# Kernel tuning notes

Measured on AMD Instinct MI355X. Metric: run time of the kernel, lower is better.

Reference implementation:

```python
import jax, jax.numpy as jnp
import numpy as np

C_IN, C_OUT = 256, 128

def setup_inputs() -> dict:
    key = jax.random.key(0)
    k1, k2, k3, k4, k5, k6 = jax.random.split(key, 6)
    B, H, W = 8, 64, 64
    p = jax.random.normal(k1, (B, C_IN, H, W), dtype=jnp.float32)
    b = jax.random.normal(k2, (B, C_IN, H, W), dtype=jnp.float32)
    # 1x1 conv weights (Conv2d with kernel 1 == pointwise matmul) + biases
    sq = 1.0 / np.sqrt(C_IN)
    Wq = jax.random.uniform(k3, (C_OUT, C_IN), jnp.float32, -sq, sq)
    bq = jax.random.uniform(k4, (C_OUT,), jnp.float32, -sq, sq)
    Wk = jax.random.uniform(k5, (C_OUT, C_IN), jnp.float32, -sq, sq)
    bk = jax.random.uniform(k6, (C_OUT,), jnp.float32, -sq, sq)
    return {"p": p, "b": b, "Wq": Wq, "bq": bq, "Wk": Wk, "bk": bk}

def reference(p, b, Wq, bq, Wk, bk):
    B, C, H, W = p.shape
    N = H * W
    # 1x1 convs -> flatten spatial dim to N
    q = jnp.einsum('bchw,oc->bhwo', p, Wq) + bq          # [B,H,W,Co]
    q = q.reshape(B, N, -1).astype(jnp.float32)           # [B,N,Co] (query permuted)
    k = jnp.einsum('bchw,oc->bohw', b, Wk) + bk[None, :, None, None]
    k = k.reshape(B, -1, N).astype(jnp.float32)           # [B,Co,N]
    energy = jnp.einsum('bnc,bcm->bnm', q, k)             # [B,N,N] unscaled
    attention = jax.nn.softmax(energy, axis=-1)           # softmax over keys
    value = b.reshape(B, C, N)                            # [B,C,N]
    out = jnp.einsum('bnm,bcm->bcn', attention, value)    # [B,C,N]
    return out.reshape(B, C, H, W)
```

## Files before the change

### kernel.cpp

```cpp
#include <hip/hip_runtime.h>
#include <hip/hip_bf16.h>
#include <math.h>


#define B_   8
#define CIN  256
#define COUT 128
#define NN   4096

typedef _Float16 half8  __attribute__((ext_vector_type(8)));
typedef short    short8 __attribute__((ext_vector_type(8)));
typedef float    f32x4  __attribute__((ext_vector_type(4)));

#define LOG2E 1.44269504088896340736f

__device__ __forceinline__ unsigned short f2bf(float f) {
    union { float f; unsigned u; } v; v.f = f;
    return (unsigned short)((v.u + 0x7FFFu + ((v.u >> 16) & 1u)) >> 16);
}
__device__ __forceinline__ unsigned short f2h(float f) {
    union { _Float16 h; unsigned short u; } v; v.h = (_Float16)f;
    return v.u;
}
__device__ __forceinline__ unsigned int cvt_pk_bf16(float lo, float hi) {
    unsigned int r;
    asm("v_cvt_pk_bf16_f32 %0, %1, %2" : "=v"(r) : "v"(lo), "v"(hi));
    return r;
}
__device__ __forceinline__ float dpp_xor1(float x) {
    union { float f; int i; } u; u.f = x;
    u.i = __builtin_amdgcn_mov_dpp(u.i, 0xB1, 0xF, 0xF, true);
    return u.f;
}
__device__ __forceinline__ void dma16(void* lds, const void* g) {
    __builtin_amdgcn_global_load_lds(
        (const __attribute__((address_space(1))) unsigned int*)g,
        (__attribute__((address_space(3))) unsigned int*)lds,
        16, 0, 0);
}

__global__ __launch_bounds__(256) void cvt_w(const float* __restrict__ Wq,
                                             const float* __restrict__ Wk,
                                             const float* __restrict__ bq,
                                             _Float16* __restrict__ Whq,
                                             _Float16* __restrict__ Whk,
                                             float* __restrict__ bqs) {
    const int bx = blockIdx.x, t = threadIdx.x;
    const int isK = (bx >= 32);
    const float* src = isK ? Wk : Wq;
    _Float16* dst = isK ? Whk : Whq;
    const float scale = isK ? 1.0f : LOG2E;
    const int idx = (bx & 31) * 256 + t;
    float4 v = ((const float4*)src)[idx];
    unsigned long long pk = (unsigned long long)f2h(v.x * scale)
                          | ((unsigned long long)f2h(v.y * scale) << 16)
                          | ((unsigned long long)f2h(v.z * scale) << 32)
                          | ((unsigned long long)f2h(v.w * scale) << 48);
    ((unsigned long long*)dst)[idx] = pk;
    if (bx == 0 && t < COUT) bqs[t] = bq[t] * LOG2E;
}

__global__ __launch_bounds__(256) void proj3(const float* __restrict__ X,
                                             const _Float16* __restrict__ Wh,
                                             const float* __restrict__ bias,
                                             _Float16* __restrict__ outN,
                                             _Float16* __restrict__ outT,
                                             unsigned short* __restrict__ Vb)
{
    __shared__ __align__(16) unsigned short T[64 * 264];
    const int bx = blockIdx.x, b = bx >> 6, n0 = (bx & 63) << 6;
    const int t  = threadIdx.x;
    const int cr = t >> 2;
    const int nch = (t & 3) << 4;

#pragma unroll
    for (int it = 0; it < 4; ++it) {
        const int c = it * 64 + cr;
        const float* src = X + ((size_t)(b * CIN + c) * NN + n0 + nch);
        float v[16];
#pragma unroll
        for (int k = 0; k < 4; ++k) {
            float4 f = *(const float4*)(src + k * 4);
            v[k*4] = f.x; v[k*4+1] = f.y; v[k*4+2] = f.z; v[k*4+3] = f.w;
        }
#pragma unroll
        for (int j = 0; j < 16; ++j) T[(nch + j) * 264 + c] = f2h(v[j]);
        if (Vb) {
            unsigned short o[16];
#pragma unroll
            for (int j = 0; j < 16; ++j) o[j] = f2bf(v[j]);
            unsigned short* dst = Vb + (size_t)(b * CIN + c) * NN + n0 + nch;
            *(int4*)dst = *(int4*)o;
            *(int4*)(dst + 8) = *(int4*)(o + 8);
        }
    }
    __syncthreads();

    const int w = t >> 6, lane = t & 63, l15 = lane & 15, quad = lane >> 4, q8 = quad * 8;
    half8 a[8];
#pragma unroll
    for (int s = 0; s < 8; ++s)
        a[s] = *(const half8*)&T[(w * 16 + l15) * 264 + s * 32 + q8];
    f32x4 D[8];
#pragma unroll
    for (int og = 0; og < 8; ++og) D[og] = (f32x4){0.f, 0.f, 0.f, 0.f};
#pragma unroll
    for (int s = 0; s < 8; ++s) {
        const _Float16* wp = Wh + (size_t)l15 * CIN + s * 32 + q8;
#pragma unroll
        for (int og = 0; og < 8; ++og) {
            half8 wf = *(const half8*)(wp + og * 16 * CIN);
            D[og] = __builtin_amdgcn_mfma_f32_16x16x32_f16(a[s], wf, D[og], 0, 0, 0);
        }
    }
    const int nrow = n0 + w * 16 + quad * 4;
    if (outT) {
#pragma unroll
        for (int og = 0; og < 8; ++og) {
            const int o = og * 16 + l15;
            const float bo = bias[o];
            const int c = o >> 3, j = o & 7;
            const int sw = (c & 7) << 2;
#pragma unroll
            for (int r2 = 0; r2 < 4; ++r2) {
                const int n = nrow + r2;
                const int tile = n >> 5, m = n & 31;
                const size_t pos = ((size_t)(b * 128 + tile) * 512
                                    + c * 32 + ((m + sw) & 31)) * 8 + j;
                outT[pos] = (_Float16)(D[og][r2] + bo);
            }
        }
    } else {
#pragma unroll
        for (int og = 0; og < 8; ++og) {
            const int o = og * 16 + l15;
            const float bo = bias[o];
            _Float16* op = outN + ((size_t)(b * NN + nrow) * COUT + o);
#pragma unroll
            for (int r2 = 0; r2 < 4; ++r2)
                op[(size_t)r2 * COUT] = (_Float16)(D[og][r2] + bo);
        }
    }
}

__global__ __launch_bounds__(256, 2) void flash_kernel(const _Float16* __restrict__ Q,
                                                       const _Float16* __restrict__ Ktt,
                                                       const unsigned short* __restrict__ V,
                                                       float* __restrict__ out) {
    __shared__ __align__(16) _Float16       K0sh[32 * 128];
    __shared__ __align__(16) _Float16       K1sh[32 * 128];
    __shared__ __align__(16) unsigned short V0sh[256 * 32];
    __shared__ __align__(16) unsigned short V1sh[256 * 32];
    __shared__ __align__(16) unsigned short V2sh[256 * 32];
    __shared__ __align__(16) unsigned short P0sh[64 * 40];
    __shared__ __align__(16) unsigned short P1sh[64 * 40];
    __shared__ __align__(16) float          Lsh[64];

    const int bx   = blockIdx.x;
    const int b    = bx >> 6;
    const int q0   = (bx & 63) << 6;
    const int t    = threadIdx.x;
    const int w    = t >> 6;
    const int lane = t & 63;
    const int l15  = lane & 15;
    const int quad = lane >> 4;
    const int q8   = quad * 8;

    const _Float16* Qg = Q + (size_t)b * NN * COUT;
    const _Float16* Kb = Ktt + (size_t)b * 128 * 4096;
    const unsigned short* Vg = V + (size_t)b * CIN * NN;

    half8 Qf[4];
    {
        const _Float16* qr = Qg + (size_t)(q0 + w * 16 + l15) * COUT;
#pragma unroll
        for (int s = 0; s < 4; ++s)
            Qf[s] = *(const half8*)(qr + s * 32 + q8);
    }

    f32x4 O[16];
#pragma unroll
    for (int i = 0; i < 16; ++i) O[i] = (f32x4){0.f, 0.f, 0.f, 0.f};
    float lsum[4] = {0.f, 0.f, 0.f, 0.f};

    const int vmq   = ((lane & 3) - ((lane >> 3) & 3)) & 3;
    const int vcrow = lane >> 2;
    const int vslot = (quad + (l15 >> 1)) & 3;

    auto issueK = [&](int kt, _Float16* Kd) {
        const _Float16* gk = Kb + (size_t)kt * 4096;
        dma16(Kd + (w * 2 + 0) * 512, gk + (w * 2 + 0) * 512 + lane * 8);
        dma16(Kd + (w * 2 + 1) * 512, gk + (w * 2 + 1) * 512 + lane * 8);
    };
    auto issueV = [&](int kt, unsigned short* Vd) {
        const int k0 = kt << 5;
#pragma unroll
        for (int i = 0; i < 4; ++i) {
            const int cc = (w * 4 + i) * 16 + vcrow;
            dma16(Vd + (w * 4 + i) * 512,
                  Vg + (size_t)cc * NN + k0 + vmq * 8);
        }
    };

    auto halfstep = [&](int kt, const _Float16* Kc, _Float16* Kn,
                        const unsigned short* Va, unsigned short* Vn2,
                        unsigned short* Pc) {
        if (kt + 1 < 128) issueK(kt + 1, Kn);

        f32x4 S0 = {0.f, 0.f, 0.f, 0.f}, S1 = {0.f, 0.f, 0.f, 0.f};
        __builtin_amdgcn_s_setprio(1);
#pragma unroll
        for (int s = 0; s < 4; ++s) {
            const int kc = 4 * s + quad;
            const int sw = (kc & 7) << 2;
            const int x0 = (l15 + sw) & 31;
            half8 kf0 = *(const half8*)(Kc + (kc * 32 + x0) * 8);
            half8 kf1 = *(const half8*)(Kc + (kc * 32 + (x0 ^ 16)) * 8);
            S0 = __builtin_amdgcn_mfma_f32_16x16x32_f16(Qf[s], kf0, S0, 0, 0, 0);
            S1 = __builtin_amdgcn_mfma_f32_16x16x32_f16(Qf[s], kf1, S1, 0, 0, 0);
        }
        __builtin_amdgcn_s_setprio(0);

        f32x4 E0, E1;
#pragma unroll
        for (int r = 0; r < 4; ++r) {
            E0[r] = exp2f(S0[r]);
            E1[r] = exp2f(S1[r]);
            lsum[r] += E0[r] + E1[r];
        }
        {
            f32x4 P0, P1;
#pragma unroll
            for (int r = 0; r < 4; ++r) { P0[r] = dpp_xor1(E0[r]); P1[r] = dpp_xor1(E1[r]); }
            const int odd = l15 & 1;
            unsigned short* wp0 = Pc + w * 640
                                + (((quad << 2) + (odd << 1)) * 40) + (l15 & ~1);
            unsigned int pk0 = cvt_pk_bf16(odd ? P0[2] : E0[0], odd ? E0[2] : P0[0]);
            unsigned int pk1 = cvt_pk_bf16(odd ? P0[3] : E0[1], odd ? E0[3] : P0[1]);
            unsigned int pk2 = cvt_pk_bf16(odd ? P1[2] : E1[0], odd ? E1[2] : P1[0]);
            unsigned int pk3 = cvt_pk_bf16(odd ? P1[3] : E1[1], odd ? E1[3] : P1[1]);
            *(unsigned int*)&wp0[0]  = pk0;
            *(unsigned int*)&wp0[40] = pk1;
            *(unsigned int*)&wp0[16] = pk2;
            *(unsigned int*)&wp0[56] = pk3;
        }

        __syncthreads();

        if (kt + 2 < 128) issueV(kt + 2, Vn2);

        {
            short8 pf[4];
#pragma unroll
            for (int ni = 0; ni < 4; ++ni)
                pf[ni] = *(const short8*)(Pc + (ni * 16 + l15) * 40 + q8);
            const unsigned short* vb = Va + (w * 64 + l15) * 32 + vslot * 8;
            __builtin_amdgcn_s_setprio(1);
#pragma unroll
            for (int cj = 0; cj < 4; ++cj) {
                short8 vf = *(const short8*)(vb + cj * 512);
#pragma unroll
                for (int ni = 0; ni < 4; ++ni)
                    O[ni * 4 + cj] = __builtin_amdgcn_mfma_f32_16x16x32_bf16(pf[ni], vf, O[ni * 4 + cj], 0, 0, 0);
            }
            __builtin_amdgcn_s_setprio(0);
        }
    };

    issueK(0, K0sh);
    issueV(0, V0sh);
    issueV(1, V1sh);
    __syncthreads();

    _Float16*       Kc = K0sh; _Float16*       Kn = K1sh;
    unsigned short* Va = V0sh; unsigned short* Vm = V1sh; unsigned short* Vn2 = V2sh;
    unsigned short* Pc = P0sh; unsigned short* Pn = P1sh;
#pragma unroll 1
    for (int kt = 0; kt < 128; ++kt) {
        halfstep(kt, Kc, Kn, Va, Vn2, Pc);
        _Float16* tk = Kc; Kc = Kn; Kn = tk;
        unsigned short* tv = Va; Va = Vm; Vm = Vn2; Vn2 = tv;
        unsigned short* tp = Pc; Pc = Pn; Pn = tp;
    }

#pragma unroll
    for (int r = 0; r < 4; ++r) {
        float s = lsum[r];
        s += __shfl_xor(s, 1);
        s += __shfl_xor(s, 2);
        s += __shfl_xor(s, 4);
        s += __shfl_xor(s, 8);
        if (l15 == 0) Lsh[w * 16 + (quad << 2) + r] = s;
    }
    __syncthreads();
    float* ob = out + (size_t)b * CIN * NN + q0;
#pragma unroll
    for (int ni = 0; ni < 4; ++ni) {
        const f32x4 lv = *(const f32x4*)&Lsh[ni * 16 + (quad << 2)];
        f32x4 linv;
#pragma unroll
        for (int r = 0; r < 4; ++r) linv[r] = 1.0f / lv[r];
        const int nb = ni * 16 + (quad << 2);
#pragma unroll
        for (int cj = 0; cj < 4; ++cj) {
            const int c = w * 64 + cj * 16 + l15;
            f32x4 val = O[ni * 4 + cj];
#pragma unroll
            for (int r = 0; r < 4; ++r) val[r] *= linv[r];
            *(f32x4*)(ob + (size_t)c * NN + nb) = val;
        }
    }
}

extern "C" void kernel_launch(void* const* d_in, const int* in_sizes, int n_in,
                              void* d_out, int out_size, void* d_ws, size_t ws_size,
                              hipStream_t stream) {
    const float* p  = (const float*)d_in[0];
    const float* bv = (const float*)d_in[1];
    const float* Wq = (const float*)d_in[2];
    const float* bq = (const float*)d_in[3];
    const float* Wk = (const float*)d_in[4];
    const float* bk = (const float*)d_in[5];
    float* outp = (float*)d_out;

    char* ws = (char*)d_ws;
    const size_t szQ = (size_t)B_ * NN * COUT * 2;
    const size_t szV = (size_t)B_ * NN * CIN * 2;
    const size_t szW = (size_t)COUT * CIN * 2;
    _Float16*       Qh  = (_Float16*)ws;
    _Float16*       Ktt = (_Float16*)(ws + szQ);
    unsigned short* Vb  = (unsigned short*)(ws + 2 * szQ);
    _Float16*       Whq = (_Float16*)(ws + 2 * szQ + szV);
    _Float16*       Whk = (_Float16*)(ws + 2 * szQ + szV + szW);
    float*          bqs = (float*)(ws + 2 * szQ + szV + 2 * szW);

    cvt_w<<<64, 256, 0, stream>>>(Wq, Wk, bq, Whq, Whk, bqs);
    proj3<<<512, 256, 0, stream>>>(p,  Whq, bqs, Qh, (_Float16*)nullptr, (unsigned short*)nullptr);
    proj3<<<512, 256, 0, stream>>>(bv, Whk, bk,  (_Float16*)nullptr, Ktt, Vb);
    flash_kernel<<<512, 256, 0, stream>>>(Qh, Ktt, Vb, outp);
}
```

Measured before the change: 284.4 us.

## Load V directly into registers, deepen K ring, stage projection stores through LDS

The flash kernel no longer DMAs V tiles into LDS. Each lane loads its V fragments straight from global memory into registers, double-buffered across two unrolled steps, while K uses a four-deep LDS ring and P uses four buffers. The projection kernel stages its outputs in LDS and writes them back with coalesced 16-byte stores, and it converts V to bf16 with the packed hardware instruction. These changes cut LDS traffic and scattered global stores, at the cost of more registers and uncoalesced per-lane V global loads.

```diff
diff --git a/kernel.cpp b/kernel.cpp
--- a/kernel.cpp
+++ b/kernel.cpp
@@ -14,10 +14,6 @@
 
 #define LOG2E 1.44269504088896340736f
 
-__device__ __forceinline__ unsigned short f2bf(float f) {
-    union { float f; unsigned u; } v; v.f = f;
-    return (unsigned short)((v.u + 0x7FFFu + ((v.u >> 16) & 1u)) >> 16);
-}
 __device__ __forceinline__ unsigned short f2h(float f) {
     union { _Float16 h; unsigned short u; } v; v.h = (_Float16)f;
     return v.u;
@@ -86,12 +82,12 @@
 #pragma unroll
         for (int j = 0; j < 16; ++j) T[(nch + j) * 264 + c] = f2h(v[j]);
         if (Vb) {
-            unsigned short o[16];
-#pragma unroll
-            for (int j = 0; j < 16; ++j) o[j] = f2bf(v[j]);
+            unsigned int o2[8];
+#pragma unroll
+            for (int j = 0; j < 8; ++j) o2[j] = cvt_pk_bf16(v[2*j], v[2*j+1]);
             unsigned short* dst = Vb + (size_t)(b * CIN + c) * NN + n0 + nch;
-            *(int4*)dst = *(int4*)o;
-            *(int4*)(dst + 8) = *(int4*)(o + 8);
+            *(int4*)dst = *(int4*)&o2[0];
+            *(int4*)(dst + 8) = *(int4*)&o2[4];
         }
     }
     __syncthreads();
@@ -113,8 +109,10 @@
             D[og] = __builtin_amdgcn_mfma_f32_16x16x32_f16(a[s], wf, D[og], 0, 0, 0);
         }
     }
-    const int nrow = n0 + w * 16 + quad * 4;
+    __syncthreads();
+
     if (outT) {
+        const int nrow = w * 16 + quad * 4;
 #pragma unroll
         for (int og = 0; og < 8; ++og) {
             const int o = og * 16 + l15;
@@ -124,22 +122,33 @@
 #pragma unroll
             for (int r2 = 0; r2 < 4; ++r2) {
                 const int n = nrow + r2;
-                const int tile = n >> 5, m = n & 31;
-                const size_t pos = ((size_t)(b * 128 + tile) * 512
-                                    + c * 32 + ((m + sw) & 31)) * 8 + j;
-                outT[pos] = (_Float16)(D[og][r2] + bo);
+                const int tl = n >> 5, m = n & 31;
+                T[tl * 4096 + (c * 32 + ((m + sw) & 31)) * 8 + j] = f2h(D[og][r2] + bo);
             }
         }
+        __syncthreads();
+        _Float16* dstk = outT + ((size_t)(b * 128 + (n0 >> 5)) * 4096 + t * 32);
+        const unsigned short* srck = T + t * 32;
+#pragma unroll
+        for (int k = 0; k < 4; ++k)
+            ((int4*)dstk)[k] = ((const int4*)srck)[k];
     } else {
+        const int nrow = w * 16 + quad * 4;
 #pragma unroll
         for (int og = 0; og < 8; ++og) {
             const int o = og * 16 + l15;
             const float bo = bias[o];
-            _Float16* op = outN + ((size_t)(b * NN + nrow) * COUT + o);
 #pragma unroll
             for (int r2 = 0; r2 < 4; ++r2)
-                op[(size_t)r2 * COUT] = (_Float16)(D[og][r2] + bo);
-        }
+                T[(nrow + r2) * 136 + o] = f2h(D[og][r2] + bo);
+        }
+        __syncthreads();
+        const int n = t >> 2, seg = t & 3;
+        const unsigned short* srcp = T + n * 136 + seg * 32;
+        _Float16* dstp = outN + ((size_t)(b * NN + n0 + n) * COUT + seg * 32);
+#pragma unroll
+        for (int k = 0; k < 4; ++k)
+            ((int4*)dstp)[k] = ((const int4*)srcp)[k];
     }
 }
 
@@ -147,13 +156,8 @@
                                                        const _Float16* __restrict__ Ktt,
                                                        const unsigned short* __restrict__ V,
                                                        float* __restrict__ out) {
-    __shared__ __align__(16) _Float16       K0sh[32 * 128];
-    __shared__ __align__(16) _Float16       K1sh[32 * 128];
-    __shared__ __align__(16) unsigned short V0sh[256 * 32];
-    __shared__ __align__(16) unsigned short V1sh[256 * 32];
-    __shared__ __align__(16) unsigned short V2sh[256 * 32];
-    __shared__ __align__(16) unsigned short P0sh[64 * 40];
-    __shared__ __align__(16) unsigned short P1sh[64 * 40];
+    __shared__ __align__(16) _Float16       Ksh[4 * 32 * 128];
+    __shared__ __align__(16) unsigned short Psh[4 * 64 * 40];
     __shared__ __align__(16) float          Lsh[64];
 
     const int bx   = blockIdx.x;
@@ -183,30 +187,23 @@
     for (int i = 0; i < 16; ++i) O[i] = (f32x4){0.f, 0.f, 0.f, 0.f};
     float lsum[4] = {0.f, 0.f, 0.f, 0.f};
 
-    const int vmq   = ((lane & 3) - ((lane >> 3) & 3)) & 3;
-    const int vcrow = lane >> 2;
-    const int vslot = (quad + (l15 >> 1)) & 3;
-
-    auto issueK = [&](int kt, _Float16* Kd) {
+    const unsigned short* Vlane = Vg + (size_t)(w * 64 + l15) * NN + q8;
+    short8 VA[4], VB[4];
+
+    auto issueK = [&](int kt) {
+        _Float16* Kd = Ksh + (size_t)(kt & 3) * 4096;
         const _Float16* gk = Kb + (size_t)kt * 4096;
         dma16(Kd + (w * 2 + 0) * 512, gk + (w * 2 + 0) * 512 + lane * 8);
         dma16(Kd + (w * 2 + 1) * 512, gk + (w * 2 + 1) * 512 + lane * 8);
     };
-    auto issueV = [&](int kt, unsigned short* Vd) {
-        const int k0 = kt << 5;
-#pragma unroll
-        for (int i = 0; i < 4; ++i) {
-            const int cc = (w * 4 + i) * 16 + vcrow;
-            dma16(Vd + (w * 4 + i) * 512,
-                  Vg + (size_t)cc * NN + k0 + vmq * 8);
-        }
+    auto loadV = [&](int kt, short8* Vd) {
+#pragma unroll
+        for (int cj = 0; cj < 4; ++cj)
+            Vd[cj] = *(const short8*)(Vlane + (size_t)cj * 16 * NN + kt * 32);
     };
 
-    auto halfstep = [&](int kt, const _Float16* Kc, _Float16* Kn,
-                        const unsigned short* Va, unsigned short* Vn2,
-                        unsigned short* Pc) {
-        if (kt + 1 < 128) issueK(kt + 1, Kn);
-
+    auto Sphase = [&](int kt, unsigned short* Pc) {
+        const _Float16* Kc = Ksh + (size_t)(kt & 3) * 4096;
         f32x4 S0 = {0.f, 0.f, 0.f, 0.f}, S1 = {0.f, 0.f, 0.f, 0.f};
         __builtin_amdgcn_s_setprio(1);
 #pragma unroll
@@ -228,59 +225,55 @@
             E1[r] = exp2f(S1[r]);
             lsum[r] += E0[r] + E1[r];
         }
-        {
-            f32x4 P0, P1;
-#pragma unroll
-            for (int r = 0; r < 4; ++r) { P0[r] = dpp_xor1(E0[r]); P1[r] = dpp_xor1(E1[r]); }
-            const int odd = l15 & 1;
-            unsigned short* wp0 = Pc + w * 640
-                                + (((quad << 2) + (odd << 1)) * 40) + (l15 & ~1);
-            unsigned int pk0 = cvt_pk_bf16(odd ? P0[2] : E0[0], odd ? E0[2] : P0[0]);
-            unsigned int pk1 = cvt_pk_bf16(odd ? P0[3] : E0[1], odd ? E0[3] : P0[1]);
-            unsigned int pk2 = cvt_pk_bf16(odd ? P1[2] : E1[0], odd ? E1[2] : P1[0]);
-            unsigned int pk3 = cvt_pk_bf16(odd ? P1[3] : E1[1], odd ? E1[3] : P1[1]);
-            *(unsigned int*)&wp0[0]  = pk0;
-            *(unsigned int*)&wp0[40] = pk1;
-            *(unsigned int*)&wp0[16] = pk2;
-            *(unsigned int*)&wp0[56] = pk3;
-        }
-
+        f32x4 P0, P1;
+#pragma unroll
+        for (int r = 0; r < 4; ++r) { P0[r] = dpp_xor1(E0[r]); P1[r] = dpp_xor1(E1[r]); }
+        const int odd = l15 & 1;
+        unsigned short* wp0 = Pc + w * 640
+                            + (((quad << 2) + (odd << 1)) * 40) + (l15 & ~1);
+        unsigned int pk0 = cvt_pk_bf16(odd ? P0[2] : E0[0], odd ? E0[2] : P0[0]);
+        unsigned int pk1 = cvt_pk_bf16(odd ? P0[3] : E0[1], odd ? E0[3] : P0[1]);
+        unsigned int pk2 = cvt_pk_bf16(odd ? P1[2] : E1[0], odd ? E1[2] : P1[0]);
+        unsigned int pk3 = cvt_pk_bf16(odd ? P1[3] : E1[1], odd ? E1[3] : P1[1]);
+        *(unsigned int*)&wp0[0]  = pk0;
+        *(unsigned int*)&wp0[40] = pk1;
+        *(unsigned int*)&wp0[16] = pk2;
+        *(unsigned int*)&wp0[56] = pk3;
+    };
+
+    auto PVphase = [&](const unsigned short* Pc, const short8* Vc) {
+        short8 pf[4];
+#pragma unroll
+        for (int ni = 0; ni < 4; ++ni)
+            pf[ni] = *(const short8*)(Pc + (ni * 16 + l15) * 40 + q8);
+        __builtin_amdgcn_s_setprio(1);
+#pragma unroll
+        for (int cj = 0; cj < 4; ++cj) {
+            short8 vf = Vc[cj];
+#pragma unroll
+            for (int ni = 0; ni < 4; ++ni)
+                O[ni * 4 + cj] = __builtin_amdgcn_mfma_f32_16x16x32_bf16(pf[ni], vf, O[ni * 4 + cj], 0, 0, 0);
+        }
+        __builtin_amdgcn_s_setprio(0);
+    };
+
+    issueK(0); issueK(1);
+    loadV(0, VA); loadV(1, VB);
+    __syncthreads();
+
+#pragma unroll 1
+    for (int kt = 0; kt < 128; kt += 2) {
+        if (kt + 2 < 128) issueK(kt + 2);
+        Sphase(kt, Psh + (size_t)(kt & 3) * 2560);
         __syncthreads();
-
-        if (kt + 2 < 128) issueV(kt + 2, Vn2);
-
-        {
-            short8 pf[4];
-#pragma unroll
-            for (int ni = 0; ni < 4; ++ni)
-                pf[ni] = *(const short8*)(Pc + (ni * 16 + l15) * 40 + q8);
-            const unsigned short* vb = Va + (w * 64 + l15) * 32 + vslot * 8;
-            __builtin_amdgcn_s_setprio(1);
-#pragma unroll
-            for (int cj = 0; cj < 4; ++cj) {
-                short8 vf = *(const short8*)(vb + cj * 512);
-#pragma unroll
-                for (int ni = 0; ni < 4; ++ni)
-                    O[ni * 4 + cj] = __builtin_amdgcn_mfma_f32_16x16x32_bf16(pf[ni], vf, O[ni * 4 + cj], 0, 0, 0);
-            }
-            __builtin_amdgcn_s_setprio(0);
-        }
-    };
-
-    issueK(0, K0sh);
-    issueV(0, V0sh);
-    issueV(1, V1sh);
-    __syncthreads();
-
-    _Float16*       Kc = K0sh; _Float16*       Kn = K1sh;
-    unsigned short* Va = V0sh; unsigned short* Vm = V1sh; unsigned short* Vn2 = V2sh;
-    unsigned short* Pc = P0sh; unsigned short* Pn = P1sh;
-#pragma unroll 1
-    for (int kt = 0; kt < 128; ++kt) {
-        halfstep(kt, Kc, Kn, Va, Vn2, Pc);
-        _Float16* tk = Kc; Kc = Kn; Kn = tk;
-        unsigned short* tv = Va; Va = Vm; Vm = Vn2; Vn2 = tv;
-        unsigned short* tp = Pc; Pc = Pn; Pn = tp;
+        PVphase(Psh + (size_t)(kt & 3) * 2560, VA);
+        if (kt + 2 < 128) loadV(kt + 2, VA);
+
+        if (kt + 3 < 128) issueK(kt + 3);
+        Sphase(kt + 1, Psh + (size_t)((kt + 1) & 3) * 2560);
+        __syncthreads();
+        PVphase(Psh + (size_t)((kt + 1) & 3) * 2560, VB);
+        if (kt + 3 < 128) loadV(kt + 3, VB);
     }
 
 #pragma unroll
```

New measurement: 304.2 us. 7.0% more time.
